# Kernel tuning notes

Measured on AMD Instinct MI355X. Metric: run time of the kernel, lower is better.

Reference implementation:

```python
import jax, jax.numpy as jnp
import numpy as np

DIM, NH = 256, 8
B, L_INNER, L_LEAF, L_ROOT = 16, 128, 64, 16


def mha(q, k, v, wi, bi, wo, bo, nh=NH):
    # Faithful torch.nn.MultiheadAttention (batch_first): packed in_proj, q scaled by head_dim**-0.5.
    E = q.shape[-1]
    hd = E // nh
    wq, wk, wv = wi[:E], wi[E:2 * E], wi[2 * E:]
    bq, bk, bv = bi[:E], bi[E:2 * E], bi[2 * E:]

    def proj(x, w, b):
        Bx, Lx, _ = x.shape
        return (x @ w.T + b).reshape(Bx, Lx, nh, hd).transpose(0, 2, 1, 3)  # [B,H,L,hd]

    qh = proj(q, wq, bq) * (float(hd) ** -0.5)
    kh = proj(k, wk, bk)
    vh = proj(v, wv, bv)
    attn = jax.nn.softmax(jnp.einsum('bhqd,bhkd->bhqk', qh, kh), axis=-1)
    o = jnp.einsum('bhqk,bhkd->bhqd', attn, vh).transpose(0, 2, 1, 3).reshape(q.shape)
    return o @ wo.T + bo


def setup_inputs() -> dict:
    key = jax.random.key(0)
    ks = jax.random.split(key, 10)
    return {
        'leaf': jax.random.normal(ks[0], (B * L_INNER, L_LEAF, DIM), jnp.float32),
        'inner': jax.random.normal(ks[1], (B, L_INNER, DIM), jnp.float32),
        'root': jax.random.normal(ks[2], (B, L_ROOT, DIM), jnp.float32),
        'w_in': jax.random.normal(ks[3], (7, 3 * DIM, DIM), jnp.float32) * 0.02,
        'b_in': jax.random.normal(ks[4], (7, 3 * DIM), jnp.float32) * 0.02,
        'w_out': jax.random.normal(ks[5], (7, DIM, DIM), jnp.float32) * 0.02,
        'b_out': jax.random.normal(ks[6], (7, DIM), jnp.float32) * 0.02,
        'weight_leaf': jax.random.normal(ks[7], (2,), jnp.float32),
        'weight_inner': jax.random.normal(ks[8], (3,), jnp.float32),
        'weight_root': jax.random.normal(ks[9], (2,), jnp.float32),
    }


def reference(leaf, inner, root, w_in, b_in, w_out, b_out, weight_leaf, weight_inner, weight_root):
    # param slots: 0 leaf_parents, 1 leaf_siblings, 2 inner_parents, 3 inner_siblings,
    #              4 inner_children, 5 root_siblings, 6 root_children (constructed but UNUSED, as in source)
    inner_flat = inner.reshape(-1, 1, DIM)  # [B*L_inner, 1, dim]

    leaf_p = mha(leaf, inner_flat, inner_flat, w_in[0], b_in[0], w_out[0], b_out[0])
    leaf_s = mha(leaf, leaf, leaf, w_in[1], b_in[1], w_out[1], b_out[1])
    wl = jax.nn.softmax(weight_leaf)
    leaf_out = wl[0] * leaf_p + wl[1] * leaf_s

    inner_p = mha(inner, root, root, w_in[2], b_in[2], w_out[2], b_out[2])
    inner_s = mha(inner, inner, inner, w_in[3], b_in[3], w_out[3], b_out[3])
    inner_c = mha(inner_flat, leaf, leaf, w_in[4], b_in[4], w_out[4], b_out[4]).reshape(inner.shape)
    wi_ = jax.nn.softmax(weight_inner)
    inner_out = wi_[0] * inner_p + wi_[1] * inner_s + wi_[2] * inner_c

    root_s = mha(root, root, root, w_in[5], b_in[5], w_out[5], b_out[5])
    # source bug reproduced: root_c also uses attn_root_siblings (slot 5)
    root_c = mha(root, inner, inner, w_in[5], b_in[5], w_out[5], b_out[5])
    wr = jax.nn.softmax(weight_root)
    root_out = wr[0] * root_s + wr[1] * root_c

    return (leaf_out, inner_out, root_out)
```

## Files before the change

### kernel.cpp

```cpp
#include <hip/hip_runtime.h>
#include <hip/hip_bf16.h>
#include <cstdint>


#define DIM 256
#define NH 8
#define HD 32

static constexpr float SCALE = 0.17677669529663687f;

typedef __bf16 bf16x8 __attribute__((ext_vector_type(8)));
typedef __bf16 bf16x4 __attribute__((ext_vector_type(4)));
typedef float  f32x4  __attribute__((ext_vector_type(4)));

__device__ __forceinline__ float dot4(const float4 a, const float4 b) {
    return a.x * b.x + a.y * b.y + a.z * b.z + a.w * b.w;
}

__global__ __launch_bounds__(256) void cvt_f2b(const float* __restrict__ s,
                                               __bf16* __restrict__ d, int n) {
    int i = (blockIdx.x * 256 + threadIdx.x) * 4;
    if (i < n) {
        float4 v = *(const float4*)(s + i);
        d[i + 0] = (__bf16)v.x; d[i + 1] = (__bf16)v.y;
        d[i + 2] = (__bf16)v.z; d[i + 3] = (__bf16)v.w;
    }
}

__device__ void mega2_body(int g,
    const float* __restrict__ X, const float* __restrict__ inner,
    const __bf16* __restrict__ W1b, const float* __restrict__ Bi1,
    const __bf16* __restrict__ W4kvb, const float* __restrict__ W4q,
    const float* __restrict__ Bi4, __bf16* __restrict__ O1,
    float* __restrict__ Oc, char* __restrict__ smem)
{
    const int xcd  = g & 7;
    const int idx  = g >> 3;
    const int b    = xcd * 256 + (idx >> 2);
    const int hg   = idx & 3;
    const int tid  = threadIdx.x;
    const int wid  = tid >> 6;
    const int lane = tid & 63;
    const int lr   = lane & 15;
    const int lk   = (lane >> 4) * 8;
    const int prow = (lane >> 4) * 4;
    const int tok0 = wid * 16 + prow;

    __bf16* Qs  = (__bf16*)smem;
    __bf16* Ks  = (__bf16*)(smem + 9216);
    __bf16* Vt  = (__bf16*)(smem + 18432);
    __bf16* K4t = (__bf16*)(smem + 27648);
    __bf16* V4t = (__bf16*)(smem + 36864);
    __bf16* Pw  = (__bf16*)(smem + 46080 + wid * 2304);
    float* qpart = (float*)(smem + 55296);
    float* qv    = qpart + 256;
    float* psm   = qv + 64;
    float* opart = psm + 128;
    __bf16* Bs  = (__bf16*)(smem + 57600);

    bf16x8 a[8];
    {
        const float* xrow = X + ((size_t)b * 64 + wid * 16 + lr) * DIM + lk;
#pragma unroll
        for (int k = 0; k < 8; ++k) {
            const f32x4 v0 = __builtin_nontemporal_load((const f32x4*)(xrow + k * 32));
            const f32x4 v1 = __builtin_nontemporal_load((const f32x4*)(xrow + k * 32 + 4));
            bf16x8 t;
            t[0] = (__bf16)v0[0]; t[1] = (__bf16)v0[1]; t[2] = (__bf16)v0[2]; t[3] = (__bf16)v0[3];
            t[4] = (__bf16)v1[0]; t[5] = (__bf16)v1[1]; t[6] = (__bf16)v1[2]; t[7] = (__bf16)v1[3];
            a[k] = t;
        }
    }

    {
        const int srow = tid >> 5;
        const int scol = (tid & 31) * 8;
        auto wsrc = [&](int t) -> const __bf16* {
            if (t < 12) {
                const int sec = t >> 2, sub = t & 3;
                return W1b + (size_t)(sec * 256 + hg * 64 + sub * 16) * DIM;
            }
            const int u = t - 12, sec = u >> 2, sub = u & 3;
            return W4kvb + (size_t)(sec * 256 + hg * 64 + sub * 16) * DIM;
        };
        {
            const __bf16* p = wsrc(0);
            bf16x8 g0 = *(const bf16x8*)(p + (size_t)srow * DIM + scol);
            bf16x8 g1 = *(const bf16x8*)(p + (size_t)(8 + srow) * DIM + scol);
            *(bf16x8*)(Bs + srow * 272 + scol) = g0;
            *(bf16x8*)(Bs + (8 + srow) * 272 + scol) = g1;
        }
        __syncthreads();

        for (int t = 0; t < 20; ++t) {
            const int cur = t & 1;
            const __bf16* Bc = Bs + cur * 4352;
            bf16x8 g0, g1;
            if (t + 1 < 20) {
                const __bf16* p = wsrc(t + 1);
                g0 = *(const bf16x8*)(p + (size_t)srow * DIM + scol);
                g1 = *(const bf16x8*)(p + (size_t)(8 + srow) * DIM + scol);
            }
            f32x4 aL = {0.f, 0.f, 0.f, 0.f}, aH = {0.f, 0.f, 0.f, 0.f};
#pragma unroll
            for (int kk = 0; kk < 4; ++kk) {
                const bf16x8 bL = *(const bf16x8*)(Bc + lr * 272 + kk * 32 + lk);
                aL = __builtin_amdgcn_mfma_f32_16x16x32_bf16(a[kk], bL, aL, 0, 0, 0);
            }
#pragma unroll
            for (int kk = 0; kk < 4; ++kk) {
                const bf16x8 bH = *(const bf16x8*)(Bc + lr * 272 + (kk + 4) * 32 + lk);
                aH = __builtin_amdgcn_mfma_f32_16x16x32_bf16(a[kk + 4], bH, aH, 0, 0, 0);
            }
            const f32x4 acc = aL + aH;
            const int sub = t & 3;
            const int col = sub * 16 + lr;
            if (t < 4) {
                const float bias = Bi1[hg * 64 + sub * 16 + lr];
#pragma unroll
                for (int r = 0; r < 4; ++r)
                    Qs[(size_t)(tok0 + r) * 72 + col] = (__bf16)((acc[r] + bias) * SCALE);
            } else if (t < 8) {
                const float bias = Bi1[256 + hg * 64 + sub * 16 + lr];
#pragma unroll
                for (int r = 0; r < 4; ++r)
                    Ks[(size_t)(tok0 + r) * 72 + col] = (__bf16)(acc[r] + bias);
            } else {
                bf16x4 pv;
                if (t < 12) {
                    const float bias = Bi1[512 + hg * 64 + sub * 16 + lr];
#pragma unroll
                    for (int r = 0; r < 4; ++r) pv[r] = (__bf16)(acc[r] + bias);
                    *(bf16x4*)(Vt + (size_t)col * 72 + tok0) = pv;
                } else if (t < 16) {
                    const float bias = Bi4[256 + hg * 64 + sub * 16 + lr];
#pragma unroll
                    for (int r = 0; r < 4; ++r) pv[r] = (__bf16)(acc[r] + bias);
                    *(bf16x4*)(K4t + (size_t)col * 72 + tok0) = pv;
                } else {
                    const float bias = Bi4[512 + hg * 64 + sub * 16 + lr];
#pragma unroll
                    for (int r = 0; r < 4; ++r) pv[r] = (__bf16)(acc[r] + bias);
                    *(bf16x4*)(V4t + (size_t)col * 72 + tok0) = pv;
                }
            }
            if (t + 1 < 20) {
                __bf16* Bn = Bs + (cur ^ 1) * 4352;
                *(bf16x8*)(Bn + srow * 272 + scol) = g0;
                *(bf16x8*)(Bn + (8 + srow) * 272 + scol) = g1;
            }
            __syncthreads();
        }
    }

    {
        const int o = tid & 63, part = tid >> 6;
        const float4* wr = (const float4*)(W4q + (size_t)(hg * 64 + o) * DIM + part * 64);
        const float4* xr = (const float4*)(inner + (size_t)b * DIM + part * 64);
        float accq = 0.f;
#pragma unroll
        for (int k = 0; k < 16; ++k) accq += dot4(xr[k], wr[k]);
        qpart[part * 64 + o] = accq;
    }
    __syncthreads();

    if (tid < 64)
        qv[tid] = (qpart[tid] + qpart[64 + tid] + qpart[128 + tid] + qpart[192 + tid]
                   + Bi4[hg * 64 + tid]) * SCALE;

    const int hh = wid >> 1;
    const int qh = wid & 1;
    f32x4 s[2][4];
    {
        bf16x8 kb[4];
#pragma unroll
        for (int kt = 0; kt < 4; ++kt)
            kb[kt] = *(const bf16x8*)(Ks + (size_t)(kt * 16 + lr) * 72 + hh * 32 + lk);
#pragma unroll
        for (int q2 = 0; q2 < 2; ++q2) {
            const int qt = qh * 2 + q2;
            const bf16x8 qa = *(const bf16x8*)(Qs + (size_t)(qt * 16 + lr) * 72 + hh * 32 + lk);
#pragma unroll
            for (int kt = 0; kt < 4; ++kt) {
                f32x4 z = {0.f, 0.f, 0.f, 0.f};
                s[q2][kt] = __builtin_amdgcn_mfma_f32_16x16x32_bf16(qa, kb[kt], z, 0, 0, 0);
            }
        }
    }
#pragma unroll
    for (int q2 = 0; q2 < 2; ++q2) {
#pragma unroll
        for (int r = 0; r < 4; ++r) {
            float m = fmaxf(fmaxf(s[q2][0][r], s[q2][1][r]), fmaxf(s[q2][2][r], s[q2][3][r]));
#pragma unroll
            for (int off = 1; off < 16; off <<= 1) m = fmaxf(m, __shfl_xor(m, off));
            const float p0 = __expf(s[q2][0][r] - m), p1 = __expf(s[q2][1][r] - m);
            const float p2 = __expf(s[q2][2][r] - m), p3 = __expf(s[q2][3][r] - m);
            float t = p0 + p1 + p2 + p3;
#pragma unroll
            for (int off = 1; off < 16; off <<= 1) t += __shfl_xor(t, off);
            const float inv = 1.0f / t;
            s[q2][0][r] = p0 * inv; s[q2][1][r] = p1 * inv;
            s[q2][2][r] = p2 * inv; s[q2][3][r] = p3 * inv;
        }
    }
    {
        bf16x8 vb[2][2];
#pragma unroll
        for (int dt = 0; dt < 2; ++dt)
#pragma unroll
            for (int ks = 0; ks < 2; ++ks)
                vb[dt][ks] = *(const bf16x8*)(Vt + (size_t)(hh * 32 + dt * 16 + lr) * 72 + ks * 32 + lk);
#pragma unroll
        for (int q2 = 0; q2 < 2; ++q2) {
            const int qt = qh * 2 + q2;
#pragma unroll
            for (int kt = 0; kt < 4; ++kt)
#pragma unroll
                for (int r = 0; r < 4; ++r)
                    Pw[(size_t)(prow + r) * 72 + kt * 16 + lr] = (__bf16)s[q2][kt][r];
            bf16x8 pa[2];
#pragma unroll
            for (int ks = 0; ks < 2; ++ks)
                pa[ks] = *(const bf16x8*)(Pw + (size_t)lr * 72 + ks * 32 + lk);
#pragma unroll
            for (int dt = 0; dt < 2; ++dt) {
                f32x4 o = {0.f, 0.f, 0.f, 0.f};
#pragma unroll
                for (int ks = 0; ks < 2; ++ks)
                    o = __builtin_amdgcn_mfma_f32_16x16x32_bf16(pa[ks], vb[dt][ks], o, 0, 0, 0);
                const int colO = (hg * 2 + hh) * 32 + dt * 16 + lr;
#pragma unroll
                for (int r = 0; r < 4; ++r)
                    __builtin_nontemporal_store((__bf16)o[r],
                        &O1[((size_t)b * 64 + qt * 16 + prow + r) * DIM + colO]);
            }
        }
    }
    __syncthreads();

    if (wid < 2) {
        const int j = lane;
        float sv = 0.f;
#pragma unroll
        for (int d = 0; d < 32; ++d)
            sv += qv[wid * 32 + d] * (float)K4t[(size_t)(wid * 32 + d) * 72 + j];
        float m = sv;
#pragma unroll
        for (int off = 1; off < 64; off <<= 1) m = fmaxf(m, __shfl_xor(m, off));
        const float p = __expf(sv - m);
        float t = p;
#pragma unroll
        for (int off = 1; off < 64; off <<= 1) t += __shfl_xor(t, off);
        psm[wid * 64 + j] = p / t;
    }
    __syncthreads();

    if (tid < 128) {
        const int o = tid & 63, hf = tid >> 6;
        const int ho = o >> 5;
        float acc2 = 0.f;
#pragma unroll
        for (int j = 0; j < 32; ++j)
            acc2 += psm[ho * 64 + hf * 32 + j] * (float)V4t[(size_t)o * 72 + hf * 32 + j];
        opart[hf * 64 + o] = acc2;
    }
    __syncthreads();
    if (tid < 64)
        Oc[(size_t)b * DIM + hg * 64 + tid] = opart[tid] + opart[64 + tid];
}

__device__ void leafp_mfma_body(int bid, const float* __restrict__ inner,
    const __bf16* __restrict__ Wv0b, const __bf16* __restrict__ Wo0b,
    const float* __restrict__ b_in0, const float* __restrict__ b_out0,
    float* __restrict__ tP, char* __restrict__ smem)
{
    __bf16* tV = (__bf16*)smem;
    __bf16* Bs = (__bf16*)(smem + 33792);
    const int tid  = threadIdx.x;
    const int wid  = tid >> 6;
    const int lane = tid & 63;
    const int lr   = lane & 15;
    const int lk   = (lane >> 4) * 8;
    const int prow = (lane >> 4) * 4;
    const int tok0 = wid * 16 + prow;
    const int srow = tid >> 5;
    const int scol = (tid & 31) * 8;

    bf16x8 a[8];
    {
        const float* xrow = inner + ((size_t)bid * 64 + wid * 16 + lr) * DIM + lk;
#pragma unroll
        for (int k = 0; k < 8; ++k) {
            float4 v0 = *(const float4*)(xrow + k * 32);
            float4 v1 = *(const float4*)(xrow + k * 32 + 4);
            bf16x8 t;
            t[0] = (__bf16)v0.x; t[1] = (__bf16)v0.y; t[2] = (__bf16)v0.z; t[3] = (__bf16)v0.w;
            t[4] = (__bf16)v1.x; t[5] = (__bf16)v1.y; t[6] = (__bf16)v1.z; t[7] = (__bf16)v1.w;
            a[k] = t;
        }
    }

    {
        bf16x8 g0 = *(const bf16x8*)(Wv0b + (size_t)srow * DIM + scol);
        bf16x8 g1 = *(const bf16x8*)(Wv0b + (size_t)(8 + srow) * DIM + scol);
        *(bf16x8*)(Bs + srow * 264 + scol) = g0;
        *(bf16x8*)(Bs + (8 + srow) * 264 + scol) = g1;
    }
    __syncthreads();
    for (int t = 0; t < 16; ++t) {
        const int cur = t & 1;
        const __bf16* Bc = Bs + cur * 4224;
        bf16x8 g0, g1;
        if (t + 1 < 16) {
            const __bf16* p = Wv0b + (size_t)((t + 1) * 16) * DIM;
            g0 = *(const bf16x8*)(p + (size_t)srow * DIM + scol);
            g1 = *(const bf16x8*)(p + (size_t)(8 + srow) * DIM + scol);
        }
        f32x4 acc = {0.f, 0.f, 0.f, 0.f};
#pragma unroll
        for (int k = 0; k < 8; ++k)
            acc = __builtin_amdgcn_mfma_f32_16x16x32_bf16(
                a[k], *(const bf16x8*)(Bc + lr * 264 + k * 32 + lk), acc, 0, 0, 0);
        const float bias = b_in0[512 + t * 16 + lr];
#pragma unroll
        for (int r = 0; r < 4; ++r)
            tV[(size_t)(tok0 + r) * 264 + t * 16 + lr] = (__bf16)(acc[r] + bias);
        if (t + 1 < 16) {
            __bf16* Bn = Bs + (cur ^ 1) * 4224;
            *(bf16x8*)(Bn + srow * 264 + scol) = g0;
            *(bf16x8*)(Bn + (8 + srow) * 264 + scol) = g1;
        }
        __syncthreads();
    }

    bf16x8 a2[8];
#pragma unroll
    for (int k = 0; k < 8; ++k)
        a2[k] = *(const bf16x8*)(tV + (size_t)(wid * 16 + lr) * 264 + k * 32 + lk);
    {
        bf16x8 g0 = *(const bf16x8*)(Wo0b + (size_t)srow * DIM + scol);
        bf16x8 g1 = *(const bf16x8*)(Wo0b + (size_t)(8 + srow) * DIM + scol);
        *(bf16x8*)(Bs + srow * 264 + scol) = g0;
        *(bf16x8*)(Bs + (8 + srow) * 264 + scol) = g1;
    }
    __syncthreads();
    for (int t = 0; t < 16; ++t) {
        const int cur = t & 1;
        const __bf16* Bc = Bs + cur * 4224;
        bf16x8 g0, g1;
        if (t + 1 < 16) {
            const __bf16* p = Wo0b + (size_t)((t + 1) * 16) * DIM;
            g0 = *(const bf16x8*)(p + (size_t)srow * DIM + scol);
            g1 = *(const bf16x8*)(p + (size_t)(8 + srow) * DIM + scol);
        }
        f32x4 acc = {0.f, 0.f, 0.f, 0.f};
#pragma unroll
        for (int k = 0; k < 8; ++k)
            acc = __builtin_amdgcn_mfma_f32_16x16x32_bf16(
                a2[k], *(const bf16x8*)(Bc + lr * 264 + k * 32 + lk), acc, 0, 0, 0);
        const float bo = b_out0[t * 16 + lr];
#pragma unroll
        for (int r = 0; r < 4; ++r)
            tP[((size_t)bid * 64 + wid * 16 + prow + r) * DIM + t * 16 + lr] = acc[r] + bo;
        if (t + 1 < 16) {
            __bf16* Bn = Bs + (cur ^ 1) * 4224;
            *(bf16x8*)(Bn + srow * 264 + scol) = g0;
            *(bf16x8*)(Bn + (8 + srow) * 264 + scol) = g1;
        }
        __syncthreads();
    }
}

template <int LQ, int LK, int RQ>
__device__ void attn_body(int bx, const float* __restrict__ Xq,
                          const float* __restrict__ Xkv,
                          const float* __restrict__ Wi, const float* __restrict__ Bi,
                          float* __restrict__ O, float* __restrict__ sm)
{
    const int b   = bx >> 3;
    const int h   = bx & 7;
    const int tid = threadIdx.x;

    float* KsP = sm;
    float* VsP = KsP + LK * 33;
    float* QsP = VsP + LK * 33;
    float* SP  = QsP + LQ * 33;

    const float* xq  = Xq  + (size_t)b * LQ * DIM;
    const float* xkv = Xkv + (size_t)b * LK * DIM;

    {
        const int col   = tid & 63;
        const int which = col >> 5;
        const int d     = col & 31;
        const int row   = DIM + which * DIM + h * HD + d;
        const float4* wr = (const float4*)(Wi + (size_t)row * DIM);
        const float bias = Bi[row];
        constexpr int TT = LK / 4;
        float acc[TT];
#pragma unroll
        for (int i = 0; i < TT; ++i) acc[i] = 0.f;
        const int t0 = tid >> 6;
        for (int k4 = 0; k4 < DIM / 4; ++k4) {
            const float4 w = wr[k4];
#pragma unroll
            for (int i = 0; i < TT; ++i) {
                const int t = t0 + 4 * i;
                const float4 aa = ((const float4*)(xkv + (size_t)t * DIM))[k4];
                acc[i] += dot4(aa, w);
            }
        }
#pragma unroll
        for (int i = 0; i < TT; ++i) {
            const int t = t0 + 4 * i;
            if (which == 0) KsP[t * 33 + d] = acc[i] + bias;
            else            VsP[t * 33 + d] = acc[i] + bias;
        }
    }
    {
        constexpr int TGQ = (LQ >= 8) ? 8 : LQ;
        constexpr int TT  = LQ / TGQ;
        if (tid < 32 * TGQ) {
            const int d   = tid & 31;
            const int row = h * HD + d;
            const float4* wr = (const float4*)(Wi + (size_t)row * DIM);
            const float bias = Bi[row];
            float acc[TT];
#pragma unroll
            for (int i = 0; i < TT; ++i) acc[i] = 0.f;
            const int t0 = tid >> 5;
            for (int k4 = 0; k4 < DIM / 4; ++k4) {
                const float4 w = wr[k4];
#pragma unroll
                for (int i = 0; i < TT; ++i) {
                    const int t = t0 + TGQ * i;
                    const float4 aa = ((const float4*)(xq + (size_t)t * DIM))[k4];
                    acc[i] += dot4(aa, w);
                }
            }
#pragma unroll
            for (int i = 0; i < TT; ++i) {
                const int t = t0 + TGQ * i;
                QsP[t * 33 + d] = (acc[i] + bias) * SCALE;
            }
        }
    }
    __syncthreads();

    for (int q0 = 0; q0 < LQ; q0 += RQ) {
        for (int idx = tid; idx < RQ * LK; idx += 256) {
            const int r = idx / LK;
            const int j = idx - r * LK;
            float acc = 0.f;
#pragma unroll
            for (int d = 0; d < HD; ++d)
                acc += QsP[(q0 + r) * 33 + d] * KsP[j * 33 + d];
            SP[r * (LK + 1) + j] = acc;
        }
        __syncthreads();
        if (tid < RQ * 8) {
            const int r   = tid >> 3;
            const int sub = tid & 7;
            float m = -1e30f;
            for (int j = sub; j < LK; j += 8) m = fmaxf(m, SP[r * (LK + 1) + j]);
#pragma unroll
            for (int off = 4; off; off >>= 1) m = fmaxf(m, __shfl_xor(m, off, 8));
            float sum = 0.f;
            for (int j = sub; j < LK; j += 8) {
                const float p = __expf(SP[r * (LK + 1) + j] - m);
                SP[r * (LK + 1) + j] = p;
                sum += p;
            }
#pragma unroll
            for (int off = 4; off; off >>= 1) sum += __shfl_xor(sum, off, 8);
            const float inv = 1.0f / sum;
            for (int j = sub; j < LK; j += 8) SP[r * (LK + 1) + j] *= inv;
        }
        __syncthreads();
        for (int idx = tid; idx < RQ * HD; idx += 256) {
            const int r = idx >> 5;
            const int d = idx & 31;
            float acc = 0.f;
            for (int j = 0; j < LK; ++j)
                acc += SP[r * (LK + 1) + j] * VsP[j * 33 + d];
            O[((size_t)(b * LQ + q0 + r)) * DIM + h * HD + d] = acc;
        }
        __syncthreads();
    }
}

__global__ __launch_bounds__(256, 2) void fused_main(
    const float* __restrict__ leaf, const float* __restrict__ inner,
    const float* __restrict__ root,
    const float* __restrict__ w_in, const float* __restrict__ b_in,
    const float* __restrict__ b_out,
    const __bf16* __restrict__ W1b, const __bf16* __restrict__ W4kvb,
    const __bf16* __restrict__ Wv0b, const __bf16* __restrict__ Wo0b,
    __bf16* __restrict__ O1, float* __restrict__ Oc, float* __restrict__ tP,
    float* __restrict__ Op, float* __restrict__ Osf,
    float* __restrict__ Ors, float* __restrict__ Orc)
{
    extern __shared__ __align__(16) char smem[];
    const int bid = blockIdx.x;
    const size_t WI = 768 * 256, BI = 768;
    if (bid < 128)
        attn_body<128, 128, 16>(bid, inner, inner, w_in + 3 * WI, b_in + 3 * BI,
                                Osf, (float*)smem);
    else if (bid < 256)
        attn_body<128, 16, 32>(bid - 128, inner, root, w_in + 2 * WI, b_in + 2 * BI,
                               Op, (float*)smem);
    else if (bid < 384)
        attn_body<16, 128, 16>(bid - 256, root, inner, w_in + 5 * WI, b_in + 5 * BI,
                               Orc, (float*)smem);
    else if (bid < 512)
        attn_body<16, 16, 16>(bid - 384, root, root, w_in + 5 * WI, b_in + 5 * BI,
                              Ors, (float*)smem);
    else if (bid < 544)
        leafp_mfma_body(bid - 512, inner, Wv0b, Wo0b, b_in, b_out, tP, smem);
    else
        mega2_body(bid - 544, leaf, inner, W1b, b_in + 1 * BI, W4kvb,
                   w_in + 4 * WI, b_in + 4 * BI, O1, Oc, smem);
}

__device__ void combleaf_body(int bid, const __bf16* __restrict__ O1,
                              const __bf16* __restrict__ Wob,
                              const float* __restrict__ Bo1,
                              const float* __restrict__ tP,
                              const float* __restrict__ wleaf,
                              float* __restrict__ out, char* __restrict__ sm)
{
    const int tid  = threadIdx.x;
    const int wid  = tid >> 6;
    const int lane = tid & 63;
    const int lr   = lane & 15;
    const int lk   = (lane >> 4) * 8;
    __bf16* Bs = (__bf16*)sm;
    const int srow = tid >> 5;
    const int scol = (tid & 31) * 8;

    bf16x8 a[8];
    {
        const __bf16* ar = O1 + ((size_t)bid * 64 + wid * 16 + lr) * DIM + lk;
#pragma unroll
        for (int k = 0; k < 8; ++k) a[k] = *(const bf16x8*)(ar + k * 32);
    }
    const float e0 = __expf(wleaf[0]), e1 = __expf(wleaf[1]);
    const float wl0 = e0 / (e0 + e1), wl1 = e1 / (e0 + e1);
    const size_t row0 = (size_t)bid * 64 + wid * 16 + (lane >> 4) * 4;

    {
        bf16x8 g0 = *(const bf16x8*)(Wob + (size_t)srow * DIM + scol);
        bf16x8 g1 = *(const bf16x8*)(Wob + (size_t)(8 + srow) * DIM + scol);
        *(bf16x8*)(Bs + srow * 272 + scol) = g0;
        *(bf16x8*)(Bs + (8 + srow) * 272 + scol) = g1;
    }
    __syncthreads();

    for (int nt = 0; nt < 16; ++nt) {
        const int cur = nt & 1;
        const __bf16* Bc = Bs + cur * 4352;
        bf16x8 g0, g1;
        if (nt + 1 < 16) {
            const __bf16* p = Wob + (size_t)((nt + 1) * 16) * DIM;
            g0 = *(const bf16x8*)(p + (size_t)srow * DIM + scol);
            g1 = *(const bf16x8*)(p + (size_t)(8 + srow) * DIM + scol);
        }
        f32x4 acc = {0.f, 0.f, 0.f, 0.f};
#pragma unroll
        for (int k = 0; k < 8; ++k)
            acc = __builtin_amdgcn_mfma_f32_16x16x32_bf16(
                a[k], *(const bf16x8*)(Bc + lr * 272 + k * 32 + lk), acc, 0, 0, 0);
        const int   o  = nt * 16 + lr;
        const float bo = Bo1[o];
        const float tv = tP[(size_t)bid * DIM + o];
#pragma unroll
        for (int r = 0; r < 4; ++r)
            out[(row0 + r) * DIM + o] = wl0 * tv + wl1 * (acc[r] + bo);
        if (nt + 1 < 16) {
            __bf16* Bn = Bs + (cur ^ 1) * 4352;
            *(bf16x8*)(Bn + srow * 272 + scol) = g0;
            *(bf16x8*)(Bn + (8 + srow) * 272 + scol) = g1;
        }
        __syncthreads();
    }
}

__device__ void combine_inner_body(int vb, const float* __restrict__ Op,
    const float* __restrict__ Osf, const float* __restrict__ Oc,
    const float* __restrict__ W2, const float* __restrict__ B2,
    const float* __restrict__ W3, const float* __restrict__ B3,
    const float* __restrict__ W4, const float* __restrict__ B4,
    const float* __restrict__ winner, float* __restrict__ out, float* __restrict__ Ts)
{
    const int n0 = vb * 32;
    const int o  = threadIdx.x;
    const float e0 = __expf(winner[0]), e1 = __expf(winner[1]), e2 = __expf(winner[2]);
    const float inv = 1.f / (e0 + e1 + e2);
    const float wt0 = e0 * inv, wt1 = e1 * inv, wt2 = e2 * inv;

    float acc[32];
#pragma unroll
    for (int r = 0; r < 32; ++r) acc[r] = 0.f;
    const float biasacc = wt0 * B2[o] + wt1 * B3[o] + wt2 * B4[o];

#pragma unroll
    for (int term = 0; term < 3; ++term) {
        const float* Ob = (term == 0) ? Op : (term == 1) ? Osf : Oc;
        const float* Wb = (term == 0) ? W2 : (term == 1) ? W3 : W4;
        const float wt  = (term == 0) ? wt0 : (term == 1) ? wt1 : wt2;
        __syncthreads();
        for (int idx = threadIdx.x; idx < 32 * DIM; idx += 256)
            Ts[idx] = Ob[(size_t)n0 * DIM + idx];
        __syncthreads();
        const float4* wr = (const float4*)(Wb + (size_t)o * DIM);
        for (int k4 = 0; k4 < DIM / 4; ++k4) {
            float4 w = wr[k4];
            w.x *= wt; w.y *= wt; w.z *= wt; w.w *= wt;
#pragma unroll
            for (int r = 0; r < 32; ++r) {
                const float4 aa = *(const float4*)&Ts[r * DIM + k4 * 4];
                acc[r] += dot4(aa, w);
            }
        }
    }
#pragma unroll
    for (int r = 0; r < 32; ++r)
        out[(size_t)(n0 + r) * DIM + o] = acc[r] + biasacc;
}

__device__ void combine_root_body(int vb, const float* __restrict__ Ors,
    const float* __restrict__ Orc, const float* __restrict__ W5,
    const float* __restrict__ B5, const float* __restrict__ wroot,
    float* __restrict__ out, float* __restrict__ Ts)
{
    const int n0 = vb * 32;
    const int o  = threadIdx.x;
    const float e0 = __expf(wroot[0]), e1 = __expf(wroot[1]);
    const float w0 = e0 / (e0 + e1), w1 = e1 / (e0 + e1);
    for (int idx = threadIdx.x; idx < 32 * DIM; idx += 256)
        Ts[idx] = w0 * Ors[(size_t)n0 * DIM + idx] + w1 * Orc[(size_t)n0 * DIM + idx];
    __syncthreads();
    float acc[32];
#pragma unroll
    for (int r = 0; r < 32; ++r) acc[r] = 0.f;
    const float4* wr = (const float4*)(W5 + (size_t)o * DIM);
    for (int k4 = 0; k4 < DIM / 4; ++k4) {
        const float4 w = wr[k4];
#pragma unroll
        for (int r = 0; r < 32; ++r) {
            const float4 aa = *(const float4*)&Ts[r * DIM + k4 * 4];
            acc[r] += dot4(aa, w);
        }
    }
    const float bo = B5[o];
#pragma unroll
    for (int r = 0; r < 32; ++r)
        out[(size_t)(n0 + r) * DIM + o] = acc[r] + bo;
}

__global__ __launch_bounds__(256) void epilogue_kernel(
    const __bf16* __restrict__ O1, const __bf16* __restrict__ Wo1b,
    const float* __restrict__ w_out, const float* __restrict__ b_out,
    const float* __restrict__ tP, const float* __restrict__ Op,
    const float* __restrict__ Osf, const float* __restrict__ Oc,
    const float* __restrict__ Ors, const float* __restrict__ Orc,
    const float* __restrict__ wleaf, const float* __restrict__ winner,
    const float* __restrict__ wroot, float* __restrict__ out)
{
    extern __shared__ float smf[];
    const int bid = blockIdx.x;
    const size_t WO = 256 * 256, BO = 256;
    if (bid < 2048)
        combleaf_body(bid, O1, Wo1b, b_out + BO, tP, wleaf, out, (char*)smf);
    else if (bid < 2112)
        combine_inner_body(bid - 2048, Op, Osf, Oc,
                           w_out + 2 * WO, b_out + 2 * BO,
                           w_out + 3 * WO, b_out + 3 * BO,
                           w_out + 4 * WO, b_out + 4 * BO,
                           winner, out + 33554432, smf);
    else
        combine_root_body(bid - 2112, Ors, Orc, w_out + 5 * WO, b_out + 5 * BO,
                          wroot, out + 33554432 + 524288, smf);
}

extern "C" void kernel_launch(void* const* d_in, const int* in_sizes, int n_in,
                              void* d_out, int out_size, void* d_ws, size_t ws_size,
                              hipStream_t stream)
{
    const float* leaf   = (const float*)d_in[0];
    const float* inner  = (const float*)d_in[1];
    const float* root   = (const float*)d_in[2];
    const float* w_in   = (const float*)d_in[3];
    const float* b_in   = (const float*)d_in[4];
    const float* w_out  = (const float*)d_in[5];
    const float* b_out  = (const float*)d_in[6];
    const float* wleaf  = (const float*)d_in[7];
    const float* winner = (const float*)d_in[8];
    const float* wroot  = (const float*)d_in[9];
    float* out = (float*)d_out;

    const size_t WI = 768 * 256, WO = 256 * 256;

    char* ws = (char*)d_ws;
    __bf16* W1b   = (__bf16*)(ws);
    __bf16* W4kvb = (__bf16*)(ws + 393216);
    __bf16* Wo1b  = (__bf16*)(ws + 655360);
    __bf16* Wv0b  = (__bf16*)(ws + 786432);
    __bf16* Wo0b  = (__bf16*)(ws + 917504);
    __bf16* O1b   = (__bf16*)(ws + 1048576);
    float*  tP    = (float*)(ws + 68157440);
    float*  Oc    = (float*)(ws + 70254592);
    float*  Op    = (float*)(ws + 72351744);
    float*  Osf   = (float*)(ws + 74448896);
    float*  Ors   = (float*)(ws + 76546048);
    float*  Orc   = (float*)(ws + 76808192);

    cvt_f2b<<<192, 256, 0, stream>>>(w_in + 1 * WI, W1b, 768 * 256);
    cvt_f2b<<<128, 256, 0, stream>>>(w_in + 4 * WI + 256 * 256, W4kvb, 512 * 256);
    cvt_f2b<<<64, 256, 0, stream>>>(w_out + 1 * WO, Wo1b, 256 * 256);
    cvt_f2b<<<64, 256, 0, stream>>>(w_in + 512 * 256, Wv0b, 256 * 256);
    cvt_f2b<<<64, 256, 0, stream>>>(w_out, Wo0b, 256 * 256);

    fused_main<<<8736, 256, 75008, stream>>>(
        leaf, inner, root, w_in, b_in, b_out, W1b, W4kvb, Wv0b, Wo0b,
        O1b, Oc, tP, Op, Osf, Ors, Orc);

    epilogue_kernel<<<2120, 256, 32768, stream>>>(O1b, Wo1b, w_out, b_out, tP,
                                                  Op, Osf, Oc, Ors, Orc,
                                                  wleaf, winner, wroot, out);
}
```

Baseline: 721.2 us.

## Stage weight tiles via direct global-to-LDS loads with XOR-swizzled layout

Pre-converts the W1 and W4 key/value weights to bf16 with an XOR swizzle of 16-byte chunks per row. The double-buffered weight staging in the projection loop now uses global_load_lds, which writes straight into LDS instead of going through registers. The old padded rows are replaced by unpadded rows, and the swizzle is there to avoid bank conflicts on the MFMA operand reads. This cuts VGPR pressure and LDS footprint slightly. The risk is correctness across the async load and the barrier, since there is no explicit vmcnt wait beyond __syncthreads.

```diff
diff --git a/kernel.cpp b/kernel.cpp
--- a/kernel.cpp
+++ b/kernel.cpp
@@ -15,6 +15,12 @@
 
 __device__ __forceinline__ float dot4(const float4 a, const float4 b) {
     return a.x * b.x + a.y * b.y + a.z * b.z + a.w * b.w;
+}
+
+__device__ __forceinline__ void gl_lds16(const void* g, void* l) {
+    __builtin_amdgcn_global_load_lds(
+        (const __attribute__((address_space(1))) void*)g,
+        (__attribute__((address_space(3))) void*)l, 16, 0, 0);
 }
 
 __global__ __launch_bounds__(256) void cvt_f2b(const float* __restrict__ s,
@@ -24,6 +30,22 @@
         float4 v = *(const float4*)(s + i);
         d[i + 0] = (__bf16)v.x; d[i + 1] = (__bf16)v.y;
         d[i + 2] = (__bf16)v.z; d[i + 3] = (__bf16)v.w;
+    }
+}
+
+__global__ __launch_bounds__(256) void cvt_f2b_swz(const float* __restrict__ s,
+                                                   __bf16* __restrict__ d, int n) {
+    int idx = blockIdx.x * 256 + threadIdx.x;
+    if (idx * 8 < n) {
+        const int r  = idx >> 5;
+        const int cs = idx & 31;
+        const float4 v0 = *(const float4*)(s + (size_t)r * 256 + cs * 8);
+        const float4 v1 = *(const float4*)(s + (size_t)r * 256 + cs * 8 + 4);
+        bf16x8 t;
+        t[0] = (__bf16)v0.x; t[1] = (__bf16)v0.y; t[2] = (__bf16)v0.z; t[3] = (__bf16)v0.w;
+        t[4] = (__bf16)v1.x; t[5] = (__bf16)v1.y; t[6] = (__bf16)v1.z; t[7] = (__bf16)v1.w;
+        const int cd = cs ^ (r & 7);
+        *(bf16x8*)(d + (size_t)r * 256 + cd * 8) = t;
     }
 }
 
@@ -73,8 +95,6 @@
     }
 
     {
-        const int srow = tid >> 5;
-        const int scol = (tid & 31) * 8;
         auto wsrc = [&](int t) -> const __bf16* {
             if (t < 12) {
                 const int sec = t >> 2, sub = t & 3;
@@ -83,33 +103,34 @@
             const int u = t - 12, sec = u >> 2, sub = u & 3;
             return W4kvb + (size_t)(sec * 256 + hg * 64 + sub * 16) * DIM;
         };
-        {
-            const __bf16* p = wsrc(0);
-            bf16x8 g0 = *(const bf16x8*)(p + (size_t)srow * DIM + scol);
-            bf16x8 g1 = *(const bf16x8*)(p + (size_t)(8 + srow) * DIM + scol);
-            *(bf16x8*)(Bs + srow * 272 + scol) = g0;
-            *(bf16x8*)(Bs + (8 + srow) * 272 + scol) = g1;
-        }
-        __syncthreads();
+        const int tid16 = tid * 16;
+        auto stage = [&](const __bf16* psrc, __bf16* Bn) {
+            const char* gp = (const char*)psrc + tid16;
+            char*       lp = (char*)Bn + tid16;
+            gl_lds16(gp, lp);
+            gl_lds16(gp + 4096, lp + 4096);
+        };
+        stage(wsrc(0), Bs);
+        __syncthreads();
+
+        const int rbase = lr * 512;
+        const int swz   = (lr & 7) << 4;
+        const int lkb   = (lane >> 4) << 4;
 
         for (int t = 0; t < 20; ++t) {
-            const int cur = t & 1;
-            const __bf16* Bc = Bs + cur * 4352;
-            bf16x8 g0, g1;
-            if (t + 1 < 20) {
-                const __bf16* p = wsrc(t + 1);
-                g0 = *(const bf16x8*)(p + (size_t)srow * DIM + scol);
-                g1 = *(const bf16x8*)(p + (size_t)(8 + srow) * DIM + scol);
-            }
+            const __bf16* Bc = Bs + (t & 1) * 4096;
+            __bf16*       Bn = Bs + ((t & 1) ^ 1) * 4096;
+            if (t + 1 < 20) stage(wsrc(t + 1), Bn);
+            const char* Bb = (const char*)Bc;
             f32x4 aL = {0.f, 0.f, 0.f, 0.f}, aH = {0.f, 0.f, 0.f, 0.f};
 #pragma unroll
             for (int kk = 0; kk < 4; ++kk) {
-                const bf16x8 bL = *(const bf16x8*)(Bc + lr * 272 + kk * 32 + lk);
+                const bf16x8 bL = *(const bf16x8*)(Bb + rbase + ((kk * 64 + lkb) ^ swz));
                 aL = __builtin_amdgcn_mfma_f32_16x16x32_bf16(a[kk], bL, aL, 0, 0, 0);
             }
 #pragma unroll
             for (int kk = 0; kk < 4; ++kk) {
-                const bf16x8 bH = *(const bf16x8*)(Bc + lr * 272 + (kk + 4) * 32 + lk);
+                const bf16x8 bH = *(const bf16x8*)(Bb + rbase + (((kk + 4) * 64 + lkb) ^ swz));
                 aH = __builtin_amdgcn_mfma_f32_16x16x32_bf16(a[kk + 4], bH, aH, 0, 0, 0);
             }
             const f32x4 acc = aL + aH;
@@ -143,11 +164,6 @@
                     for (int r = 0; r < 4; ++r) pv[r] = (__bf16)(acc[r] + bias);
                     *(bf16x4*)(V4t + (size_t)col * 72 + tok0) = pv;
                 }
-            }
-            if (t + 1 < 20) {
-                __bf16* Bn = Bs + (cur ^ 1) * 4352;
-                *(bf16x8*)(Bn + srow * 272 + scol) = g0;
-                *(bf16x8*)(Bn + (8 + srow) * 272 + scol) = g1;
             }
             __syncthreads();
         }
@@ -716,13 +732,13 @@
     float*  Ors   = (float*)(ws + 76546048);
     float*  Orc   = (float*)(ws + 76808192);
 
-    cvt_f2b<<<192, 256, 0, stream>>>(w_in + 1 * WI, W1b, 768 * 256);
-    cvt_f2b<<<128, 256, 0, stream>>>(w_in + 4 * WI + 256 * 256, W4kvb, 512 * 256);
+    cvt_f2b_swz<<<96, 256, 0, stream>>>(w_in + 1 * WI, W1b, 768 * 256);
+    cvt_f2b_swz<<<64, 256, 0, stream>>>(w_in + 4 * WI + 256 * 256, W4kvb, 512 * 256);
     cvt_f2b<<<64, 256, 0, stream>>>(w_out + 1 * WO, Wo1b, 256 * 256);
     cvt_f2b<<<64, 256, 0, stream>>>(w_in + 512 * 256, Wv0b, 256 * 256);
     cvt_f2b<<<64, 256, 0, stream>>>(w_out, Wo0b, 256 * 256);
 
-    fused_main<<<8736, 256, 75008, stream>>>(
+    fused_main<<<8736, 256, 73984, stream>>>(
         leaf, inner, root, w_in, b_in, b_out, W1b, W4kvb, Wv0b, Wo0b,
         O1b, Oc, tP, Op, Osf, Ors, Orc);
 
```

New measurement: 733.3 us. No clear change (+1.7%).

## Stage X tile in LDS, split weight tiles across waves, split leaf out-proj kernel

Applied to the files above, without the earlier changes.

In the mega2 projection, the 64-token X tile is now converted to bf16 once into LDS. Each wave owns five of the twenty weight column tiles and reads them straight from global memory into registers, with a prefetch for the next tile. This removes the per-tile shared weight staging and the twenty block-wide barriers, at the cost of more LDS and register pressure. The leaf output projection moves into its own 512-thread kernel that loads the whole Wo1 matrix into LDS once and handles 128 rows per block, and the remaining combines go to a smaller kernel. The larger LDS footprint (79872 bytes in the main kernel, 135168 in the new one) may lower occupancy.

```diff
diff --git a/kernel.cpp b/kernel.cpp
--- a/kernel.cpp
+++ b/kernel.cpp
@@ -44,37 +44,35 @@
     const int lr   = lane & 15;
     const int lk   = (lane >> 4) * 8;
     const int prow = (lane >> 4) * 4;
-    const int tok0 = wid * 16 + prow;
-
-    __bf16* Qs  = (__bf16*)smem;
-    __bf16* Ks  = (__bf16*)(smem + 9216);
-    __bf16* Vt  = (__bf16*)(smem + 18432);
-    __bf16* K4t = (__bf16*)(smem + 27648);
-    __bf16* V4t = (__bf16*)(smem + 36864);
-    __bf16* Pw  = (__bf16*)(smem + 46080 + wid * 2304);
-    float* qpart = (float*)(smem + 55296);
+
+    __bf16* Xs  = (__bf16*)smem;
+    __bf16* Pw  = (__bf16*)(smem + wid * 2304);
+    float* qpart = (float*)(smem + 9216);
     float* qv    = qpart + 256;
     float* psm   = qv + 64;
     float* opart = psm + 128;
-    __bf16* Bs  = (__bf16*)(smem + 57600);
-
-    bf16x8 a[8];
-    {
-        const float* xrow = X + ((size_t)b * 64 + wid * 16 + lr) * DIM + lk;
-#pragma unroll
-        for (int k = 0; k < 8; ++k) {
-            const f32x4 v0 = __builtin_nontemporal_load((const f32x4*)(xrow + k * 32));
-            const f32x4 v1 = __builtin_nontemporal_load((const f32x4*)(xrow + k * 32 + 4));
-            bf16x8 t;
-            t[0] = (__bf16)v0[0]; t[1] = (__bf16)v0[1]; t[2] = (__bf16)v0[2]; t[3] = (__bf16)v0[3];
-            t[4] = (__bf16)v1[0]; t[5] = (__bf16)v1[1]; t[6] = (__bf16)v1[2]; t[7] = (__bf16)v1[3];
-            a[k] = t;
-        }
-    }
-
-    {
-        const int srow = tid >> 5;
-        const int scol = (tid & 31) * 8;
+    __bf16* Qs  = (__bf16*)(smem + 33792);
+    __bf16* Ks  = (__bf16*)(smem + 43008);
+    __bf16* Vt  = (__bf16*)(smem + 52224);
+    __bf16* K4t = (__bf16*)(smem + 61440);
+    __bf16* V4t = (__bf16*)(smem + 70656);
+
+    {
+        const float* xb = X + (size_t)b * 64 * DIM;
+#pragma unroll
+        for (int it = 0; it < 16; ++it) {
+            const int e4 = it * 1024 + tid * 4;
+            const f32x4 v = __builtin_nontemporal_load((const f32x4*)(xb + e4));
+            bf16x4 t4;
+            t4[0] = (__bf16)v[0]; t4[1] = (__bf16)v[1];
+            t4[2] = (__bf16)v[2]; t4[3] = (__bf16)v[3];
+            const int row = e4 >> 8, col = e4 & 255;
+            *(bf16x4*)(Xs + row * 264 + col) = t4;
+        }
+    }
+    __syncthreads();
+
+    {
         auto wsrc = [&](int t) -> const __bf16* {
             if (t < 12) {
                 const int sec = t >> 2, sub = t & 3;
@@ -83,75 +81,87 @@
             const int u = t - 12, sec = u >> 2, sub = u & 3;
             return W4kvb + (size_t)(sec * 256 + hg * 64 + sub * 16) * DIM;
         };
+        const size_t boff = (size_t)lr * DIM + lk;
+        const int t0w = wid * 5;
+        bf16x8 bw[8], bn[8];
         {
-            const __bf16* p = wsrc(0);
-            bf16x8 g0 = *(const bf16x8*)(p + (size_t)srow * DIM + scol);
-            bf16x8 g1 = *(const bf16x8*)(p + (size_t)(8 + srow) * DIM + scol);
-            *(bf16x8*)(Bs + srow * 272 + scol) = g0;
-            *(bf16x8*)(Bs + (8 + srow) * 272 + scol) = g1;
-        }
-        __syncthreads();
-
-        for (int t = 0; t < 20; ++t) {
-            const int cur = t & 1;
-            const __bf16* Bc = Bs + cur * 4352;
-            bf16x8 g0, g1;
-            if (t + 1 < 20) {
-                const __bf16* p = wsrc(t + 1);
-                g0 = *(const bf16x8*)(p + (size_t)srow * DIM + scol);
-                g1 = *(const bf16x8*)(p + (size_t)(8 + srow) * DIM + scol);
-            }
-            f32x4 aL = {0.f, 0.f, 0.f, 0.f}, aH = {0.f, 0.f, 0.f, 0.f};
-#pragma unroll
-            for (int kk = 0; kk < 4; ++kk) {
-                const bf16x8 bL = *(const bf16x8*)(Bc + lr * 272 + kk * 32 + lk);
-                aL = __builtin_amdgcn_mfma_f32_16x16x32_bf16(a[kk], bL, aL, 0, 0, 0);
-            }
-#pragma unroll
-            for (int kk = 0; kk < 4; ++kk) {
-                const bf16x8 bH = *(const bf16x8*)(Bc + lr * 272 + (kk + 4) * 32 + lk);
-                aH = __builtin_amdgcn_mfma_f32_16x16x32_bf16(a[kk + 4], bH, aH, 0, 0, 0);
-            }
-            const f32x4 acc = aL + aH;
+            const __bf16* p = wsrc(t0w) + boff;
+#pragma unroll
+            for (int kk = 0; kk < 8; ++kk) bw[kk] = *(const bf16x8*)(p + kk * 32);
+        }
+        for (int i = 0; i < 5; ++i) {
+            const int t = t0w + i;
+            if (i + 1 < 5) {
+                const __bf16* p = wsrc(t + 1) + boff;
+#pragma unroll
+                for (int kk = 0; kk < 8; ++kk) bn[kk] = *(const bf16x8*)(p + kk * 32);
+            }
+            f32x4 acc0 = {0.f,0.f,0.f,0.f}, acc1 = {0.f,0.f,0.f,0.f};
+            f32x4 acc2 = {0.f,0.f,0.f,0.f}, acc3 = {0.f,0.f,0.f,0.f};
+#pragma unroll
+            for (int kk = 0; kk < 8; ++kk) {
+                const size_t ko = (size_t)kk * 32 + lk;
+                const bf16x8 a0 = *(const bf16x8*)(Xs + (size_t)(lr)      * 264 + ko);
+                const bf16x8 a1 = *(const bf16x8*)(Xs + (size_t)(16 + lr) * 264 + ko);
+                const bf16x8 a2 = *(const bf16x8*)(Xs + (size_t)(32 + lr) * 264 + ko);
+                const bf16x8 a3 = *(const bf16x8*)(Xs + (size_t)(48 + lr) * 264 + ko);
+                acc0 = __builtin_amdgcn_mfma_f32_16x16x32_bf16(a0, bw[kk], acc0, 0, 0, 0);
+                acc1 = __builtin_amdgcn_mfma_f32_16x16x32_bf16(a1, bw[kk], acc1, 0, 0, 0);
+                acc2 = __builtin_amdgcn_mfma_f32_16x16x32_bf16(a2, bw[kk], acc2, 0, 0, 0);
+                acc3 = __builtin_amdgcn_mfma_f32_16x16x32_bf16(a3, bw[kk], acc3, 0, 0, 0);
+            }
+            f32x4 accT[4] = { acc0, acc1, acc2, acc3 };
             const int sub = t & 3;
             const int col = sub * 16 + lr;
             if (t < 4) {
                 const float bias = Bi1[hg * 64 + sub * 16 + lr];
 #pragma unroll
-                for (int r = 0; r < 4; ++r)
-                    Qs[(size_t)(tok0 + r) * 72 + col] = (__bf16)((acc[r] + bias) * SCALE);
+                for (int tg = 0; tg < 4; ++tg)
+#pragma unroll
+                    for (int r = 0; r < 4; ++r)
+                        Qs[(size_t)(tg * 16 + prow + r) * 72 + col] =
+                            (__bf16)((accT[tg][r] + bias) * SCALE);
             } else if (t < 8) {
                 const float bias = Bi1[256 + hg * 64 + sub * 16 + lr];
 #pragma unroll
-                for (int r = 0; r < 4; ++r)
-                    Ks[(size_t)(tok0 + r) * 72 + col] = (__bf16)(acc[r] + bias);
+                for (int tg = 0; tg < 4; ++tg)
+#pragma unroll
+                    for (int r = 0; r < 4; ++r)
+                        Ks[(size_t)(tg * 16 + prow + r) * 72 + col] =
+                            (__bf16)(accT[tg][r] + bias);
+            } else if (t < 12) {
+                const float bias = Bi1[512 + hg * 64 + sub * 16 + lr];
+#pragma unroll
+                for (int tg = 0; tg < 4; ++tg) {
+                    bf16x4 pv;
+#pragma unroll
+                    for (int r = 0; r < 4; ++r) pv[r] = (__bf16)(accT[tg][r] + bias);
+                    *(bf16x4*)(Vt + (size_t)col * 72 + tg * 16 + prow) = pv;
+                }
+            } else if (t < 16) {
+                const float bias = Bi4[256 + hg * 64 + sub * 16 + lr];
+#pragma unroll
+                for (int tg = 0; tg < 4; ++tg) {
+                    bf16x4 pv;
+#pragma unroll
+                    for (int r = 0; r < 4; ++r) pv[r] = (__bf16)(accT[tg][r] + bias);
+                    *(bf16x4*)(K4t + (size_t)col * 72 + tg * 16 + prow) = pv;
+                }
             } else {
-                bf16x4 pv;
-                if (t < 12) {
-                    const float bias = Bi1[512 + hg * 64 + sub * 16 + lr];
-#pragma unroll
-                    for (int r = 0; r < 4; ++r) pv[r] = (__bf16)(acc[r] + bias);
-                    *(bf16x4*)(Vt + (size_t)col * 72 + tok0) = pv;
-                } else if (t < 16) {
-                    const float bias = Bi4[256 + hg * 64 + sub * 16 + lr];
-#pragma unroll
-                    for (int r = 0; r < 4; ++r) pv[r] = (__bf16)(acc[r] + bias);
-                    *(bf16x4*)(K4t + (size_t)col * 72 + tok0) = pv;
-                } else {
-                    const float bias = Bi4[512 + hg * 64 + sub * 16 + lr];
-#pragma unroll
-                    for (int r = 0; r < 4; ++r) pv[r] = (__bf16)(acc[r] + bias);
-                    *(bf16x4*)(V4t + (size_t)col * 72 + tok0) = pv;
+                const float bias = Bi4[512 + hg * 64 + sub * 16 + lr];
+#pragma unroll
+                for (int tg = 0; tg < 4; ++tg) {
+                    bf16x4 pv;
+#pragma unroll
+                    for (int r = 0; r < 4; ++r) pv[r] = (__bf16)(accT[tg][r] + bias);
+                    *(bf16x4*)(V4t + (size_t)col * 72 + tg * 16 + prow) = pv;
                 }
             }
-            if (t + 1 < 20) {
-                __bf16* Bn = Bs + (cur ^ 1) * 4352;
-                *(bf16x8*)(Bn + srow * 272 + scol) = g0;
-                *(bf16x8*)(Bn + (8 + srow) * 272 + scol) = g1;
-            }
-            __syncthreads();
-        }
-    }
+#pragma unroll
+            for (int kk = 0; kk < 8; ++kk) bw[kk] = bn[kk];
+        }
+    }
+    __syncthreads();
 
     {
         const int o = tid & 63, part = tid >> 6;
@@ -523,66 +533,55 @@
                    w_in + 4 * WI, b_in + 4 * BI, O1, Oc, smem);
 }
 
-__device__ void combleaf_body(int bid, const __bf16* __restrict__ O1,
-                              const __bf16* __restrict__ Wob,
-                              const float* __restrict__ Bo1,
-                              const float* __restrict__ tP,
-                              const float* __restrict__ wleaf,
-                              float* __restrict__ out, char* __restrict__ sm)
-{
+__global__ __launch_bounds__(512) void combleaf_kernel(
+    const __bf16* __restrict__ O1, const __bf16* __restrict__ Wo1,
+    const float* __restrict__ Bo1, const float* __restrict__ tP,
+    const float* __restrict__ wleaf, float* __restrict__ out)
+{
+    extern __shared__ __align__(16) char smem[];
+    __bf16* Ws = (__bf16*)smem;
+    const int bid  = blockIdx.x;
     const int tid  = threadIdx.x;
     const int wid  = tid >> 6;
     const int lane = tid & 63;
     const int lr   = lane & 15;
     const int lk   = (lane >> 4) * 8;
-    __bf16* Bs = (__bf16*)sm;
-    const int srow = tid >> 5;
-    const int scol = (tid & 31) * 8;
+    const int prow = (lane >> 4) * 4;
 
     bf16x8 a[8];
     {
-        const __bf16* ar = O1 + ((size_t)bid * 64 + wid * 16 + lr) * DIM + lk;
+        const __bf16* ar = O1 + ((size_t)bid * 128 + wid * 16 + lr) * DIM + lk;
 #pragma unroll
         for (int k = 0; k < 8; ++k) a[k] = *(const bf16x8*)(ar + k * 32);
     }
+    {
+        const int row = tid >> 1, hf = tid & 1;
+        const __bf16* p = Wo1 + (size_t)row * DIM + hf * 128;
+        __bf16* dst = Ws + (size_t)row * 264 + hf * 128;
+#pragma unroll
+        for (int q = 0; q < 16; ++q)
+            *(bf16x8*)(dst + q * 8) = *(const bf16x8*)(p + q * 8);
+    }
+    __syncthreads();
+
     const float e0 = __expf(wleaf[0]), e1 = __expf(wleaf[1]);
     const float wl0 = e0 / (e0 + e1), wl1 = e1 / (e0 + e1);
-    const size_t row0 = (size_t)bid * 64 + wid * 16 + (lane >> 4) * 4;
-
-    {
-        bf16x8 g0 = *(const bf16x8*)(Wob + (size_t)srow * DIM + scol);
-        bf16x8 g1 = *(const bf16x8*)(Wob + (size_t)(8 + srow) * DIM + scol);
-        *(bf16x8*)(Bs + srow * 272 + scol) = g0;
-        *(bf16x8*)(Bs + (8 + srow) * 272 + scol) = g1;
-    }
-    __syncthreads();
+    const int   tile = bid * 2 + (wid >> 2);
+    const size_t row0 = (size_t)bid * 128 + wid * 16 + prow;
 
     for (int nt = 0; nt < 16; ++nt) {
-        const int cur = nt & 1;
-        const __bf16* Bc = Bs + cur * 4352;
-        bf16x8 g0, g1;
-        if (nt + 1 < 16) {
-            const __bf16* p = Wob + (size_t)((nt + 1) * 16) * DIM;
-            g0 = *(const bf16x8*)(p + (size_t)srow * DIM + scol);
-            g1 = *(const bf16x8*)(p + (size_t)(8 + srow) * DIM + scol);
-        }
         f32x4 acc = {0.f, 0.f, 0.f, 0.f};
 #pragma unroll
         for (int k = 0; k < 8; ++k)
             acc = __builtin_amdgcn_mfma_f32_16x16x32_bf16(
-                a[k], *(const bf16x8*)(Bc + lr * 272 + k * 32 + lk), acc, 0, 0, 0);
+                a[k], *(const bf16x8*)(Ws + (size_t)(nt * 16 + lr) * 264 + k * 32 + lk),
+                acc, 0, 0, 0);
         const int   o  = nt * 16 + lr;
         const float bo = Bo1[o];
-        const float tv = tP[(size_t)bid * DIM + o];
+        const float tv = tP[(size_t)tile * DIM + o];
 #pragma unroll
         for (int r = 0; r < 4; ++r)
             out[(row0 + r) * DIM + o] = wl0 * tv + wl1 * (acc[r] + bo);
-        if (nt + 1 < 16) {
-            __bf16* Bn = Bs + (cur ^ 1) * 4352;
-            *(bf16x8*)(Bn + srow * 272 + scol) = g0;
-            *(bf16x8*)(Bn + (8 + srow) * 272 + scol) = g1;
-        }
-        __syncthreads();
     }
 }
 
@@ -659,28 +658,24 @@
         out[(size_t)(n0 + r) * DIM + o] = acc[r] + bo;
 }
 
-__global__ __launch_bounds__(256) void epilogue_kernel(
-    const __bf16* __restrict__ O1, const __bf16* __restrict__ Wo1b,
+__global__ __launch_bounds__(256) void combine_kernel(
     const float* __restrict__ w_out, const float* __restrict__ b_out,
-    const float* __restrict__ tP, const float* __restrict__ Op,
-    const float* __restrict__ Osf, const float* __restrict__ Oc,
-    const float* __restrict__ Ors, const float* __restrict__ Orc,
-    const float* __restrict__ wleaf, const float* __restrict__ winner,
+    const float* __restrict__ Op, const float* __restrict__ Osf,
+    const float* __restrict__ Oc, const float* __restrict__ Ors,
+    const float* __restrict__ Orc, const float* __restrict__ winner,
     const float* __restrict__ wroot, float* __restrict__ out)
 {
     extern __shared__ float smf[];
     const int bid = blockIdx.x;
     const size_t WO = 256 * 256, BO = 256;
-    if (bid < 2048)
-        combleaf_body(bid, O1, Wo1b, b_out + BO, tP, wleaf, out, (char*)smf);
-    else if (bid < 2112)
-        combine_inner_body(bid - 2048, Op, Osf, Oc,
+    if (bid < 64)
+        combine_inner_body(bid, Op, Osf, Oc,
                            w_out + 2 * WO, b_out + 2 * BO,
                            w_out + 3 * WO, b_out + 3 * BO,
                            w_out + 4 * WO, b_out + 4 * BO,
                            winner, out + 33554432, smf);
     else
-        combine_root_body(bid - 2112, Ors, Orc, w_out + 5 * WO, b_out + 5 * BO,
+        combine_root_body(bid - 64, Ors, Orc, w_out + 5 * WO, b_out + 5 * BO,
                           wroot, out + 33554432 + 524288, smf);
 }
 
@@ -722,11 +717,12 @@
     cvt_f2b<<<64, 256, 0, stream>>>(w_in + 512 * 256, Wv0b, 256 * 256);
     cvt_f2b<<<64, 256, 0, stream>>>(w_out, Wo0b, 256 * 256);
 
-    fused_main<<<8736, 256, 75008, stream>>>(
+    fused_main<<<8736, 256, 79872, stream>>>(
         leaf, inner, root, w_in, b_in, b_out, W1b, W4kvb, Wv0b, Wo0b,
         O1b, Oc, tP, Op, Osf, Ors, Orc);
 
-    epilogue_kernel<<<2120, 256, 32768, stream>>>(O1b, Wo1b, w_out, b_out, tP,
-                                                  Op, Osf, Oc, Ors, Orc,
-                                                  wleaf, winner, wroot, out);
-}
+    combleaf_kernel<<<1024, 512, 135168, stream>>>(O1b, Wo1b, b_out + 256, tP,
+                                                   wleaf, out);
+    combine_kernel<<<72, 256, 32768, stream>>>(w_out, b_out, Op, Osf, Oc,
+                                               Ors, Orc, winner, wroot, out);
+}
```

New measurement: 727.9 us. No clear change (+0.9%).
